# Optimization experiments

Measured on AMD Instinct MI355X. Metric: run time of the kernel, lower is better.

Reference implementation:

```python
import jax, jax.numpy as jnp
import numpy as np

B, S, H, E = 8, 2048, 1024, 8
CAP_FACTOR = 1.25  # deepspeed-style capacity factor for top-1 gating


def setup_inputs() -> dict:
    key = jax.random.key(0)
    ks = jax.random.split(key, 10)
    sc = 0.02
    return {
        "x": jax.random.normal(ks[0], (B, S, H), jnp.float32),
        "W_in": jax.random.normal(ks[1], (H, H), jnp.float32) * sc,
        "b_in": jnp.zeros((H,), jnp.float32),
        "W_gate": jax.random.normal(ks[2], (H, E), jnp.float32) * sc,
        "W1": jax.random.normal(ks[3], (E, H, H), jnp.float32) * sc,
        "b1": jnp.zeros((E, H), jnp.float32),
        "W2": jax.random.normal(ks[4], (E, H, H), jnp.float32) * sc,
        "b2": jnp.zeros((E, H), jnp.float32),
        "Wr1": jax.random.normal(ks[5], (H, H), jnp.float32) * sc,
        "br1": jnp.zeros((H,), jnp.float32),
        "Wr2": jax.random.normal(ks[6], (H, H), jnp.float32) * sc,
        "br2": jnp.zeros((H,), jnp.float32),
        "W_coef": jax.random.normal(ks[7], (H, 2), jnp.float32) * sc,
        "b_coef": jnp.zeros((2,), jnp.float32),
        "W_out": jax.random.normal(ks[8], (H, H), jnp.float32) * sc,
        "b_out": jnp.zeros((H,), jnp.float32),
    }


def _moe(x, W_gate, W1, b1, W2, b2, Wr1, br1, Wr2, br2, W_coef, b_coef):
    # x: [T, H] flattened tokens. Top-1 gating with capacity dropping + residual expert.
    T, Hd = x.shape
    nE = W_gate.shape[1]
    cap = int(np.ceil(CAP_FACTOR * T / nE))  # static under jit

    gates = jax.nn.softmax(x @ W_gate)                  # [T, E]
    eidx = jnp.argmax(gates, axis=-1)                    # [T]
    mask1 = jax.nn.one_hot(eidx, nE, dtype=x.dtype)      # [T, E]
    pos = jnp.cumsum(mask1, axis=0) - 1.0                # position within each expert
    pos_tok = jnp.take_along_axis(pos, eidx[:, None], 1)[:, 0].astype(jnp.int32)
    keep = (pos_tok < cap).astype(x.dtype)               # capacity drop mask
    gate_val = jnp.take_along_axis(gates, eidx[:, None], 1)[:, 0] * keep  # [T]
    slot = jnp.minimum(pos_tok, cap - 1)                 # safe slot index

    # scatter tokens into [E, cap, H] buffers (dropped tokens contribute zeros)
    disp = jnp.zeros((nE, cap, Hd), x.dtype).at[eidx, slot].add(x * keep[:, None])
    h = jax.nn.relu(jnp.einsum('ech,ehf->ecf', disp, W1) + b1[:, None, :])
    eo = jnp.einsum('ecf,efg->ecg', h, W2) + b2[:, None, :]
    moe_out = eo[eidx, slot] * gate_val[:, None]         # gather back; dropped -> 0

    # residual expert on all tokens, mixed with learned 2-way softmax coefficient
    res = jax.nn.relu(x @ Wr1 + br1) @ Wr2 + br2
    coef = jax.nn.softmax(x @ W_coef + b_coef)           # [T, 2]
    return moe_out * coef[:, :1] + res * coef[:, 1:]


def reference(x, W_in, b_in, W_gate, W1, b1, W2, b2, Wr1, br1, Wr2, br2,
              W_coef, b_coef, W_out, b_out):
    Bb, Ss, Hd = x.shape
    t = x.reshape(-1, Hd) @ W_in + b_in
    t = _moe(t, W_gate, W1, b1, W2, b2, Wr1, br1, Wr2, br2, W_coef, b_coef)
    t = t @ W_out + b_out
    return t.reshape(Bb, Ss, Hd)
```

## Files before the change

kernel.cpp:

```cpp
#include <hip/hip_runtime.h>
#include <cstdint>

#define T_TOK 16384
#define HD    1024
#define NE    8
#define CAP   2560
#define NCHUNK (T_TOK / 64)

typedef __attribute__((ext_vector_type(4))) float f32x4;
typedef __attribute__((ext_vector_type(8))) short bf16x8;

__device__ __forceinline__ unsigned short f2bf(float f) {
    union { float f; unsigned u; } x{f};
    unsigned r = x.u + 0x7FFF + ((x.u >> 16) & 1);
    return (unsigned short)(r >> 16);
}

__device__ __forceinline__ void gload_lds16(const unsigned short* g, unsigned short* l) {
    __builtin_amdgcn_global_load_lds(
        (const __attribute__((address_space(1))) void*)g,
        (__attribute__((address_space(3))) void*)l, 16, 0, 0);
}

template<bool GATHER, bool RELU, bool ROWSCALE, bool SCATTER, bool OUTBF16>
__global__ __launch_bounds__(512)
void gemm_bf16_k(const unsigned short* __restrict__ A,
                 const unsigned short* __restrict__ Bt,
                 const float* __restrict__ bias,
                 void* __restrict__ Cv,
                 int M, int N, int K,
                 const int* __restrict__ idxTab,
                 const float* __restrict__ rs,
                 const float* __restrict__ post,
                 long aB, long bB, long biasB, long tabB, long cB)
{
    const int nx = gridDim.x, ny = gridDim.y;
    long nwg = (long)nx * ny * gridDim.z;
    long flat = blockIdx.x + (long)nx * (blockIdx.y + (long)ny * blockIdx.z);
    long cpx = nwg >> 3;
    long swz = (flat & 7) * cpx + (flat >> 3);
    const int bx = (int)(swz % nx);
    const int by = (int)((swz / nx) % ny);
    const int bz = (int)(swz / ((long)nx * ny));

    A  += (long)bz * aB;
    Bt += (long)bz * bB;
    const float* bptr = bias ? bias + (long)bz * biasB : nullptr;
    const int* tab = idxTab ? idxTab + (long)bz * tabB : nullptr;
    float*          Cf = (float*)Cv + (long)bz * cB;
    unsigned short* Cb = (unsigned short*)Cv + (long)bz * cB;

    const int m0 = by * 256, n0 = bx * 128;

    if ((GATHER || SCATTER) && tab[m0] < 0) return;

    __shared__ unsigned short As[256][64];
    __shared__ unsigned short Bs[128][64];

    const int tid  = threadIdx.x;
    const int wv   = tid >> 6;
    const int lane = tid & 63;

    const int srow = lane >> 3;
    const int schk = lane & 7;

    const unsigned short* aSrc[4];
    const unsigned short* bSrc[2];
    #pragma unroll
    for (int i = 0; i < 4; ++i) {
        int lrow = wv * 32 + i * 8 + srow;
        int scol = ((schk ^ (lrow & 7)) * 8);
        long sr;
        if (GATHER) { int tr = tab[m0 + lrow]; sr = tr < 0 ? 0 : tr; }
        else        sr = m0 + lrow;
        aSrc[i] = A + sr * (long)K + scol;
    }
    #pragma unroll
    for (int i = 0; i < 2; ++i) {
        int lrow = wv * 16 + i * 8 + srow;
        int scol = ((schk ^ (lrow & 7)) * 8);
        bSrc[i] = Bt + (long)(n0 + lrow) * K + scol;
    }

    f32x4 acc[4][4] = {};
    const int wm = wv >> 1, wn = wv & 1;
    const int fr = lane & 15, kg = lane >> 4;

    for (int k0 = 0; k0 < K; k0 += 64) {
        __syncthreads();
        #pragma unroll
        for (int i = 0; i < 4; ++i)
            gload_lds16(aSrc[i] + k0, &As[wv * 32 + i * 8][0]);
        #pragma unroll
        for (int i = 0; i < 2; ++i)
            gload_lds16(bSrc[i] + k0, &Bs[wv * 16 + i * 8][0]);
        __syncthreads();

        #pragma unroll
        for (int kk = 0; kk < 2; ++kk) {
            bf16x8 af[4], bfr[4];
            #pragma unroll
            for (int i2 = 0; i2 < 4; ++i2) {
                int R = wm * 64 + i2 * 16 + fr;
                af[i2] = *(const bf16x8*)&As[R][((kk * 4 + kg) ^ (R & 7)) * 8];
            }
            #pragma unroll
            for (int j2 = 0; j2 < 4; ++j2) {
                int R = wn * 64 + j2 * 16 + fr;
                bfr[j2] = *(const bf16x8*)&Bs[R][((kk * 4 + kg) ^ (R & 7)) * 8];
            }
            #pragma unroll
            for (int i2 = 0; i2 < 4; ++i2)
                #pragma unroll
                for (int j2 = 0; j2 < 4; ++j2)
                    acc[i2][j2] = __builtin_amdgcn_mfma_f32_16x16x32_bf16(
                        af[i2], bfr[j2], acc[i2][j2], 0, 0, 0);
        }
    }

    const int colL = lane & 15, rgrp = (lane >> 4) * 4;
    #pragma unroll
    for (int i2 = 0; i2 < 4; ++i2) {
        #pragma unroll
        for (int r = 0; r < 4; ++r) {
            int gm = m0 + wm * 64 + i2 * 16 + rgrp + r;
            int token = gm; float sc = 1.0f;
            if (SCATTER) {
                token = tab[gm];
                if (token < 0) continue;
                sc = rs[token];
            } else if (ROWSCALE) {
                sc = rs[gm];
            }
            #pragma unroll
            for (int j2 = 0; j2 < 4; ++j2) {
                int gn = n0 + wn * 64 + j2 * 16 + colL;
                float v = acc[i2][j2][r] + (bptr ? bptr[gn] : 0.0f);
                if (RELU) v = fmaxf(v, 0.0f);
                if (SCATTER) {
                    Cf[(long)token * N + gn] += v * sc;
                } else {
                    if (ROWSCALE) {
                        v = v * sc + (post ? post[gn] : 0.0f);
                    }
                    if (OUTBF16) Cb[(long)gm * N + gn] = f2bf(v);
                    else         Cf[(long)gm * N + gn] = v;
                }
            }
        }
    }
}

__global__ __launch_bounds__(256)
void cast_bf16_k(const float* __restrict__ in, unsigned short* __restrict__ out,
                 long n4)
{
    long i = (long)blockIdx.x * 256 + threadIdx.x;
    long stride = (long)gridDim.x * 256;
    for (; i < n4; i += stride) {
        float4 v = ((const float4*)in)[i];
        ushort4 o;
        o.x = f2bf(v.x); o.y = f2bf(v.y); o.z = f2bf(v.z); o.w = f2bf(v.w);
        ((ushort4*)out)[i] = o;
    }
}

__global__ __launch_bounds__(256)
void transpose_cast_k(const float* __restrict__ W, unsigned short* __restrict__ Wt,
                      int K, int N, long wB, long wtB)
{
    const int z = blockIdx.z;
    W  += (long)z * wB;
    Wt += (long)z * wtB;
    __shared__ float tile[64][65];
    const int k0 = blockIdx.x * 64, n0 = blockIdx.y * 64;
    const int c = threadIdx.x & 63, r4 = threadIdx.x >> 6;
    #pragma unroll 4
    for (int it = 0; it < 16; ++it) {
        int row = it * 4 + r4;
        tile[row][c] = W[(long)(k0 + row) * N + n0 + c];
    }
    __syncthreads();
    #pragma unroll 4
    for (int it = 0; it < 16; ++it) {
        int nrow = it * 4 + r4;
        Wt[(long)(n0 + nrow) * K + k0 + c] = f2bf(tile[c][nrow]);
    }
}

__global__ void vecmat_init_k(const float* __restrict__ badd, long bB,
                              float* __restrict__ out, long oB)
{
    const int z = blockIdx.y;
    const int n = blockIdx.x * 256 + threadIdx.x;
    out[z * oB + n] = badd ? badd[z * bB + n] : 0.0f;
}

__global__ void vecmat_acc_k(const float* __restrict__ v, long vB,
                             const float* __restrict__ W, long wB,
                             float* __restrict__ out, long oB)
{
    const int z = blockIdx.z;
    const int n = blockIdx.x * 256 + threadIdx.x;
    const int kc = blockIdx.y;
    const float* vp = v + z * vB;
    const float* Wp = W + z * wB;
    float acc = 0.f;
    #pragma unroll 8
    for (int k = kc * 128; k < kc * 128 + 128; ++k)
        acc = fmaf(vp[k], Wp[(long)k * HD + n], acc);
    atomicAdd(out + z * oB + n, acc);
}

__global__ __launch_bounds__(256)
void wsmall_k(const float* __restrict__ W_in, const float* __restrict__ W_gate,
              const float* __restrict__ W_coef,
              float* __restrict__ wgp, float* __restrict__ wcp)
{
    const int r = blockIdx.x * 4 + (threadIdx.x >> 6);
    const int lane = threadIdx.x & 63;
    float s[10] = {};
    for (int k = lane; k < HD; k += 64) {
        float a = W_in[(long)r * HD + k];
        const float4* g = (const float4*)(W_gate + (long)k * 8);
        float4 g0 = g[0], g1 = g[1];
        s[0] += a * g0.x; s[1] += a * g0.y; s[2] += a * g0.z; s[3] += a * g0.w;
        s[4] += a * g1.x; s[5] += a * g1.y; s[6] += a * g1.z; s[7] += a * g1.w;
        float2 cv = *(const float2*)(W_coef + (long)k * 2);
        s[8] += a * cv.x; s[9] += a * cv.y;
    }
    #pragma unroll
    for (int off = 32; off > 0; off >>= 1)
        #pragma unroll
        for (int e = 0; e < 10; ++e) s[e] += __shfl_xor(s[e], off);
    if (lane == 0) {
        #pragma unroll
        for (int e = 0; e < 8; ++e) wgp[(long)r * 8 + e] = s[e];
        wcp[(long)r * 2 + 0] = s[8];
        wcp[(long)r * 2 + 1] = s[9];
    }
}

__global__ void gbias_k(const float* __restrict__ b_in, const float* __restrict__ W_gate,
                        const float* __restrict__ W_coef, const float* __restrict__ b_coef,
                        float* __restrict__ bg, float* __restrict__ bc)
{
    const int lane = threadIdx.x;
    float s[10] = {};
    for (int k = lane; k < HD; k += 64) {
        float a = b_in[k];
        const float4* g = (const float4*)(W_gate + (long)k * 8);
        float4 g0 = g[0], g1 = g[1];
        s[0] += a * g0.x; s[1] += a * g0.y; s[2] += a * g0.z; s[3] += a * g0.w;
        s[4] += a * g1.x; s[5] += a * g1.y; s[6] += a * g1.z; s[7] += a * g1.w;
        float2 cv = *(const float2*)(W_coef + (long)k * 2);
        s[8] += a * cv.x; s[9] += a * cv.y;
    }
    #pragma unroll
    for (int off = 32; off > 0; off >>= 1)
        #pragma unroll
        for (int e = 0; e < 10; ++e) s[e] += __shfl_xor(s[e], off);
    if (lane == 0) {
        #pragma unroll
        for (int e = 0; e < 8; ++e) bg[e] = s[e];
        bc[0] = s[8] + b_coef[0];
        bc[1] = s[9] + b_coef[1];
    }
}

__global__ __launch_bounds__(256)
void gating_k(const float* __restrict__ x,
              const float* __restrict__ Wg,
              const float* __restrict__ Wc,
              const float* __restrict__ bg,
              const float* __restrict__ bc,
              unsigned short* __restrict__ xb,
              int* __restrict__ eidx,
              float* __restrict__ gval,
              float* __restrict__ coef0,
              float* __restrict__ coef1)
{
    const int tok = (blockIdx.x * 256 + threadIdx.x) >> 6;
    const int lane = threadIdx.x & 63;
    const float* row = x + (long)tok * HD;
    unsigned short* orow = xb + (long)tok * HD;

    float acc[8] = {};
    float c0 = 0.f, c1 = 0.f;
    for (int i = 0; i < HD / 64; ++i) {
        int k = i * 64 + lane;
        float tv = row[k];
        orow[k] = f2bf(tv);
        const float4* wg = (const float4*)(Wg + (long)k * 8);
        float4 w0 = wg[0], w1 = wg[1];
        acc[0] = fmaf(tv, w0.x, acc[0]); acc[1] = fmaf(tv, w0.y, acc[1]);
        acc[2] = fmaf(tv, w0.z, acc[2]); acc[3] = fmaf(tv, w0.w, acc[3]);
        acc[4] = fmaf(tv, w1.x, acc[4]); acc[5] = fmaf(tv, w1.y, acc[5]);
        acc[6] = fmaf(tv, w1.z, acc[6]); acc[7] = fmaf(tv, w1.w, acc[7]);
        float2 wcv = *(const float2*)(Wc + (long)k * 2);
        c0 = fmaf(tv, wcv.x, c0);
        c1 = fmaf(tv, wcv.y, c1);
    }
    #pragma unroll
    for (int off = 32; off > 0; off >>= 1) {
        #pragma unroll
        for (int e = 0; e < 8; ++e) acc[e] += __shfl_xor(acc[e], off);
        c0 += __shfl_xor(c0, off);
        c1 += __shfl_xor(c1, off);
    }
    if (lane == 0) {
        #pragma unroll
        for (int e = 0; e < 8; ++e) acc[e] += bg[e];
        float m = acc[0]; int best = 0;
        #pragma unroll
        for (int e = 1; e < 8; ++e) if (acc[e] > m) { m = acc[e]; best = e; }
        float s = 0.f;
        #pragma unroll
        for (int e = 0; e < 8; ++e) s += expf(acc[e] - m);
        eidx[tok] = best;
        gval[tok] = 1.0f / s;
        float l0 = c0 + bc[0], l1 = c1 + bc[1];
        float mm = fmaxf(l0, l1);
        float e0 = expf(l0 - mm), e1 = expf(l1 - mm);
        float inv = 1.0f / (e0 + e1);
        coef0[tok] = e0 * inv;
        coef1[tok] = e1 * inv;
    }
}

__global__ void scan_hist_k(const int* __restrict__ eidx,
                            int* __restrict__ counts,
                            int* __restrict__ idxTab)
{
    const int b = blockIdx.x;
    const int lane = threadIdx.x;
    for (int j = b * 64 + lane; j < NE * CAP; j += NCHUNK * 64)
        idxTab[j] = -1;
    int e = eidx[b * 64 + lane];
    #pragma unroll
    for (int ex = 0; ex < NE; ++ex) {
        unsigned long long msk = __ballot(e == ex);
        if (lane == ex) counts[b * NE + ex] = (int)__popcll(msk);
    }
}

__global__ void scan_offsets_k(const int* __restrict__ counts,
                               int* __restrict__ offsets)
{
    const int e = threadIdx.x;
    if (e < NE) {
        int run = 0;
        for (int b = 0; b < NCHUNK; ++b) {
            offsets[b * NE + e] = run;
            run += counts[b * NE + e];
        }
    }
}

__global__ void scan_fill_k(const int* __restrict__ eidx,
                            const float* __restrict__ gval,
                            const float* __restrict__ coef0,
                            const int* __restrict__ offsets,
                            int* __restrict__ idxTab,
                            float* __restrict__ smoe)
{
    const int b = blockIdx.x;
    const int lane = threadIdx.x;
    const int tok = b * 64 + lane;
    int e = eidx[tok];
    unsigned long long below = (lane == 0) ? 0ull : ((~0ull) >> (64 - lane));
    int myrank = 0;
    #pragma unroll
    for (int ex = 0; ex < NE; ++ex) {
        unsigned long long msk = __ballot(e == ex);
        if (e == ex) myrank = (int)__popcll(msk & below) + offsets[b * NE + ex];
    }
    if (myrank < CAP) {
        idxTab[e * CAP + myrank] = tok;
        smoe[tok] = gval[tok] * coef0[tok];
    } else {
        smoe[tok] = 0.0f;
    }
}

extern "C" void kernel_launch(void* const* d_in, const int* in_sizes, int n_in,
                              void* d_out, int out_size, void* d_ws, size_t ws_size,
                              hipStream_t stream)
{
    const float* x      = (const float*)d_in[0];
    const float* W_in   = (const float*)d_in[1];
    const float* b_in   = (const float*)d_in[2];
    const float* W_gate = (const float*)d_in[3];
    const float* W1     = (const float*)d_in[4];
    const float* b1     = (const float*)d_in[5];
    const float* W2     = (const float*)d_in[6];
    const float* b2     = (const float*)d_in[7];
    const float* Wr1    = (const float*)d_in[8];
    const float* br1    = (const float*)d_in[9];
    const float* Wr2    = (const float*)d_in[10];
    const float* br2    = (const float*)d_in[11];
    const float* W_coef = (const float*)d_in[12];
    const float* b_coef = (const float*)d_in[13];
    const float* W_out  = (const float*)d_in[14];
    const float* b_out  = (const float*)d_in[15];
    float* out = (float*)d_out;

    const size_t MiB = 1024 * 1024;
    char* ws = (char*)d_ws;
    unsigned short* W1T   = (unsigned short*)(ws + 0);
    unsigned short* Wr1T  = (unsigned short*)(ws + 16 * MiB);
    unsigned short* Winp  = (unsigned short*)(ws + 18 * MiB);
    unsigned short* Wr2p  = (unsigned short*)(ws + 20 * MiB);
    unsigned short* W2p   = (unsigned short*)(ws + 22 * MiB);
    unsigned short* WoutT = (unsigned short*)(ws + 38 * MiB);
    unsigned short* h     = (unsigned short*)(ws + 0);
    unsigned short* WF1T  = (unsigned short*)(ws + 40 * MiB);
    unsigned short* WFr1T = (unsigned short*)(ws + 56 * MiB);
    unsigned short* WFr2T = (unsigned short*)(ws + 58 * MiB);
    unsigned short* WF2T  = (unsigned short*)(ws + 60 * MiB);
    unsigned short* res1  = (unsigned short*)(ws + 76 * MiB);
    char* sm = ws + 108 * MiB;
    float* wgp  = (float*)(sm);            sm += HD * 8 * 4;
    float* wcp  = (float*)(sm);            sm += HD * 2 * 4;
    float* bg   = (float*)(sm);            sm += 64;
    float* bc   = (float*)(sm);            sm += 64;
    float* bf1  = (float*)(sm);            sm += NE * HD * 4;
    float* bfr1 = (float*)(sm);            sm += HD * 4;
    float* c2   = (float*)(sm);            sm += HD * 4;
    float* c3   = (float*)(sm);            sm += NE * HD * 4;
    int*   eidx = (int*)(sm);              sm += T_TOK * 4;
    float* gval = (float*)(sm);            sm += T_TOK * 4;
    float* cf0  = (float*)(sm);            sm += T_TOK * 4;
    float* cf1  = (float*)(sm);            sm += T_TOK * 4;
    float* smoe = (float*)(sm);            sm += T_TOK * 4;
    int* idxTab = (int*)(sm);              sm += NE * CAP * 4;
    int* counts = (int*)(sm);              sm += NCHUNK * NE * 4;
    int* offs   = (int*)(sm);              sm += NCHUNK * NE * 4;
    unsigned short* xb = (unsigned short*)d_out;
    (void)ws_size; (void)in_sizes; (void)n_in; (void)out_size;

    const long HD2 = (long)HD * HD;
    dim3 blk(256);
    dim3 blkG(512);
    dim3 gT(16, 16, 1);
    dim3 gT8(16, 16, 8);
    dim3 gBig(HD / 128, T_TOK / 256, 1);
    dim3 gExp(HD / 128, CAP / 256, NE);
    dim3 gFuse(HD / 128, HD / 256, 9);

    transpose_cast_k<<<gT8, blk, 0, stream>>>(W1, W1T, HD, HD, HD2, HD2);
    transpose_cast_k<<<gT,  blk, 0, stream>>>(Wr1,   Wr1T,  HD, HD, 0, 0);
    transpose_cast_k<<<gT,  blk, 0, stream>>>(W_out, WoutT, HD, HD, 0, 0);
    cast_bf16_k<<<512,  blk, 0, stream>>>(W_in, Winp, HD2 / 4);
    cast_bf16_k<<<512,  blk, 0, stream>>>(Wr2,  Wr2p, HD2 / 4);
    cast_bf16_k<<<2048, blk, 0, stream>>>(W2,   W2p,  (long)NE * HD2 / 4);
    wsmall_k<<<HD / 4, blk, 0, stream>>>(W_in, W_gate, W_coef, wgp, wcp);
    gbias_k<<<1, 64, 0, stream>>>(b_in, W_gate, W_coef, b_coef, bg, bc);
    { dim3 gi(HD / 256, NE), ga(HD / 256, NE, NE);
      vecmat_init_k<<<dim3(HD/256, NE), blk, 0, stream>>>(b1, HD, bf1, HD);
      vecmat_acc_k <<<dim3(HD/256, 8, NE), blk, 0, stream>>>(b_in, 0, W1, HD2, bf1, HD);
      vecmat_init_k<<<dim3(HD/256, 1), blk, 0, stream>>>(br1, 0, bfr1, 0);
      vecmat_acc_k <<<dim3(HD/256, 8, 1), blk, 0, stream>>>(b_in, 0, Wr1, 0, bfr1, 0);
      vecmat_init_k<<<dim3(HD/256, 1), blk, 0, stream>>>(nullptr, 0, c2, 0);
      vecmat_acc_k <<<dim3(HD/256, 8, 1), blk, 0, stream>>>(br2, 0, W_out, 0, c2, 0);
      vecmat_init_k<<<dim3(HD/256, NE), blk, 0, stream>>>(nullptr, 0, c3, HD);
      vecmat_acc_k <<<dim3(HD/256, 8, NE), blk, 0, stream>>>(b2, HD, W_out, 0, c3, HD);
    }
    gating_k<<<T_TOK / 4, blk, 0, stream>>>(x, wgp, wcp, bg, bc, xb,
                                            eidx, gval, cf0, cf1);
    scan_hist_k<<<NCHUNK, 64, 0, stream>>>(eidx, counts, idxTab);
    scan_offsets_k<<<1, 64, 0, stream>>>(counts, offs);
    scan_fill_k<<<NCHUNK, 64, 0, stream>>>(eidx, gval, cf0, offs, idxTab, smoe);
    gemm_bf16_k<false, false, false, false, true><<<gFuse, blkG, 0, stream>>>(
        W1T, Winp, nullptr, WF1T, HD, HD, HD, nullptr, nullptr, nullptr,
        HD2, 0, 0, 0, HD2);
    gemm_bf16_k<false, false, false, false, true><<<gFuse, blkG, 0, stream>>>(
        WoutT, Wr2p, nullptr, WFr2T, HD, HD, HD, nullptr, nullptr, nullptr,
        0, HD2, 0, 0, HD2);
    gemm_bf16_k<true, true, false, false, true><<<gExp, blkG, 0, stream>>>(
        xb, WF1T, bf1, h, CAP, HD, HD, idxTab, nullptr, nullptr,
        0, HD2, HD, CAP, (long)CAP * HD);
    gemm_bf16_k<false, true, false, false, true><<<gBig, blkG, 0, stream>>>(
        xb, WFr1T, bfr1, res1, T_TOK, HD, HD, nullptr, nullptr, nullptr,
        0, 0, 0, 0, 0);
    gemm_bf16_k<false, false, true, false, false><<<gBig, blkG, 0, stream>>>(
        res1, WFr2T, c2, out, T_TOK, HD, HD, nullptr, cf1, b_out,
        0, 0, 0, 0, 0);
    gemm_bf16_k<false, false, false, true, false><<<gExp, blkG, 0, stream>>>(
        h, WF2T, c3, out, CAP, HD, HD, idxTab, smoe, nullptr,
        (long)CAP * HD, HD2, HD, CAP, 0);
}
```

Measured before the change: 459.9 us.

## Unfold W_out from expert and residual weights; apply a separate output GEMM

Stops pre-multiplying W2 and Wr2 by W_out, which removes the 9-batch weight-fusion GEMM and the bias-folding vecmat kernels. The residual GEMM now writes a coefficient-scaled fp32 mix into the output buffer. The expert scatter GEMM adds its result to that mix and writes a bf16 copy, and a small kernel casts capacity-dropped tokens, collected through an atomic drop list. A final token-by-H GEMM with W_out then produces the output. This has more FLOPs than the folded weights and adds an extra pass over activations, in exchange for fewer preprocessing kernels and keeping W_out unfused, which may also improve numerical accuracy.

```diff
diff --git a/kernel.cpp b/kernel.cpp
--- a/kernel.cpp
+++ b/kernel.cpp
@@ -31,7 +31,7 @@
                  int M, int N, int K,
                  const int* __restrict__ idxTab,
                  const float* __restrict__ rs,
-                 const float* __restrict__ post,
+                 const float* __restrict__ addsrc,
                  long aB, long bB, long biasB, long tabB, long cB)
 {
     const int nx = gridDim.x, ny = gridDim.y;
@@ -138,16 +138,33 @@
                 float v = acc[i2][j2][r] + (bptr ? bptr[gn] : 0.0f);
                 if (RELU) v = fmaxf(v, 0.0f);
                 if (SCATTER) {
-                    Cf[(long)token * N + gn] += v * sc;
+                    long idx = (long)token * N + gn;
+                    if (OUTBF16) Cb[idx] = f2bf(addsrc[idx] + v * sc);
+                    else         Cf[idx] += v * sc;
                 } else {
-                    if (ROWSCALE) {
-                        v = v * sc + (post ? post[gn] : 0.0f);
-                    }
+                    if (ROWSCALE) v *= sc;
                     if (OUTBF16) Cb[(long)gm * N + gn] = f2bf(v);
                     else         Cf[(long)gm * N + gn] = v;
                 }
             }
         }
+    }
+}
+
+__global__ __launch_bounds__(256)
+void drop_cast_k(const float* __restrict__ mix, unsigned short* __restrict__ mixb,
+                 const int* __restrict__ droplist, const int* __restrict__ dropcnt)
+{
+    const int cnt = *dropcnt;
+    for (int i = blockIdx.x; i < cnt; i += gridDim.x) {
+        const int tok = droplist[i];
+        const float4* src = (const float4*)(mix + (long)tok * HD);
+        ushort4* dst = (ushort4*)(mixb + (long)tok * HD);
+        const int j = threadIdx.x;
+        float4 v = src[j];
+        ushort4 o;
+        o.x = f2bf(v.x); o.y = f2bf(v.y); o.z = f2bf(v.z); o.w = f2bf(v.w);
+        dst[j] = o;
     }
 }
 
@@ -345,9 +362,11 @@
 }
 
 __global__ void scan_offsets_k(const int* __restrict__ counts,
-                               int* __restrict__ offsets)
+                               int* __restrict__ offsets,
+                               int* __restrict__ dropcnt)
 {
     const int e = threadIdx.x;
+    if (e == 63) *dropcnt = 0;
     if (e < NE) {
         int run = 0;
         for (int b = 0; b < NCHUNK; ++b) {
@@ -362,7 +381,9 @@
                             const float* __restrict__ coef0,
                             const int* __restrict__ offsets,
                             int* __restrict__ idxTab,
-                            float* __restrict__ smoe)
+                            float* __restrict__ smoe,
+                            int* __restrict__ droplist,
+                            int* __restrict__ dropcnt)
 {
     const int b = blockIdx.x;
     const int lane = threadIdx.x;
@@ -380,6 +401,8 @@
         smoe[tok] = gval[tok] * coef0[tok];
     } else {
         smoe[tok] = 0.0f;
+        int di = atomicAdd(dropcnt, 1);
+        droplist[di] = tok;
     }
 }
 
@@ -410,24 +433,21 @@
     unsigned short* W1T   = (unsigned short*)(ws + 0);
     unsigned short* Wr1T  = (unsigned short*)(ws + 16 * MiB);
     unsigned short* Winp  = (unsigned short*)(ws + 18 * MiB);
-    unsigned short* Wr2p  = (unsigned short*)(ws + 20 * MiB);
-    unsigned short* W2p   = (unsigned short*)(ws + 22 * MiB);
-    unsigned short* WoutT = (unsigned short*)(ws + 38 * MiB);
     unsigned short* h     = (unsigned short*)(ws + 0);
     unsigned short* WF1T  = (unsigned short*)(ws + 40 * MiB);
     unsigned short* WFr1T = (unsigned short*)(ws + 56 * MiB);
-    unsigned short* WFr2T = (unsigned short*)(ws + 58 * MiB);
-    unsigned short* WF2T  = (unsigned short*)(ws + 60 * MiB);
-    unsigned short* res1  = (unsigned short*)(ws + 76 * MiB);
-    char* sm = ws + 108 * MiB;
+    unsigned short* W2T   = (unsigned short*)(ws + 58 * MiB);
+    unsigned short* Wr2T  = (unsigned short*)(ws + 74 * MiB);
+    unsigned short* WoutT = (unsigned short*)(ws + 76 * MiB);
+    unsigned short* res1  = (unsigned short*)(ws + 78 * MiB);
+    unsigned short* mixb  = (unsigned short*)(ws + 78 * MiB);
+    char* sm = ws + 110 * MiB;
     float* wgp  = (float*)(sm);            sm += HD * 8 * 4;
     float* wcp  = (float*)(sm);            sm += HD * 2 * 4;
     float* bg   = (float*)(sm);            sm += 64;
     float* bc   = (float*)(sm);            sm += 64;
     float* bf1  = (float*)(sm);            sm += NE * HD * 4;
     float* bfr1 = (float*)(sm);            sm += HD * 4;
-    float* c2   = (float*)(sm);            sm += HD * 4;
-    float* c3   = (float*)(sm);            sm += NE * HD * 4;
     int*   eidx = (int*)(sm);              sm += T_TOK * 4;
     float* gval = (float*)(sm);            sm += T_TOK * 4;
     float* cf0  = (float*)(sm);            sm += T_TOK * 4;
@@ -436,7 +456,10 @@
     int* idxTab = (int*)(sm);              sm += NE * CAP * 4;
     int* counts = (int*)(sm);              sm += NCHUNK * NE * 4;
     int* offs   = (int*)(sm);              sm += NCHUNK * NE * 4;
+    int* droplist = (int*)(sm);            sm += T_TOK * 4;
+    int* dropcnt  = (int*)(sm);            sm += 64;
     unsigned short* xb = (unsigned short*)d_out;
+    float* mix = out;
     (void)ws_size; (void)in_sizes; (void)n_in; (void)out_size;
 
     const long HD2 = (long)HD * HD;
@@ -450,33 +473,25 @@
 
     transpose_cast_k<<<gT8, blk, 0, stream>>>(W1, W1T, HD, HD, HD2, HD2);
     transpose_cast_k<<<gT,  blk, 0, stream>>>(Wr1,   Wr1T,  HD, HD, 0, 0);
+    transpose_cast_k<<<gT8, blk, 0, stream>>>(W2, W2T, HD, HD, HD2, HD2);
+    transpose_cast_k<<<gT,  blk, 0, stream>>>(Wr2,   Wr2T,  HD, HD, 0, 0);
     transpose_cast_k<<<gT,  blk, 0, stream>>>(W_out, WoutT, HD, HD, 0, 0);
-    cast_bf16_k<<<512,  blk, 0, stream>>>(W_in, Winp, HD2 / 4);
-    cast_bf16_k<<<512,  blk, 0, stream>>>(Wr2,  Wr2p, HD2 / 4);
-    cast_bf16_k<<<2048, blk, 0, stream>>>(W2,   W2p,  (long)NE * HD2 / 4);
+    cast_bf16_k<<<512, blk, 0, stream>>>(W_in, Winp, HD2 / 4);
     wsmall_k<<<HD / 4, blk, 0, stream>>>(W_in, W_gate, W_coef, wgp, wcp);
     gbias_k<<<1, 64, 0, stream>>>(b_in, W_gate, W_coef, b_coef, bg, bc);
-    { dim3 gi(HD / 256, NE), ga(HD / 256, NE, NE);
-      vecmat_init_k<<<dim3(HD/256, NE), blk, 0, stream>>>(b1, HD, bf1, HD);
-      vecmat_acc_k <<<dim3(HD/256, 8, NE), blk, 0, stream>>>(b_in, 0, W1, HD2, bf1, HD);
-      vecmat_init_k<<<dim3(HD/256, 1), blk, 0, stream>>>(br1, 0, bfr1, 0);
-      vecmat_acc_k <<<dim3(HD/256, 8, 1), blk, 0, stream>>>(b_in, 0, Wr1, 0, bfr1, 0);
-      vecmat_init_k<<<dim3(HD/256, 1), blk, 0, stream>>>(nullptr, 0, c2, 0);
-      vecmat_acc_k <<<dim3(HD/256, 8, 1), blk, 0, stream>>>(br2, 0, W_out, 0, c2, 0);
-      vecmat_init_k<<<dim3(HD/256, NE), blk, 0, stream>>>(nullptr, 0, c3, HD);
-      vecmat_acc_k <<<dim3(HD/256, 8, NE), blk, 0, stream>>>(b2, HD, W_out, 0, c3, HD);
-    }
+    vecmat_init_k<<<dim3(HD/256, NE), blk, 0, stream>>>(b1, HD, bf1, HD);
+    vecmat_acc_k <<<dim3(HD/256, 8, NE), blk, 0, stream>>>(b_in, 0, W1, HD2, bf1, HD);
+    vecmat_init_k<<<dim3(HD/256, 1), blk, 0, stream>>>(br1, 0, bfr1, 0);
+    vecmat_acc_k <<<dim3(HD/256, 8, 1), blk, 0, stream>>>(b_in, 0, Wr1, 0, bfr1, 0);
     gating_k<<<T_TOK / 4, blk, 0, stream>>>(x, wgp, wcp, bg, bc, xb,
                                             eidx, gval, cf0, cf1);
     scan_hist_k<<<NCHUNK, 64, 0, stream>>>(eidx, counts, idxTab);
-    scan_offsets_k<<<1, 64, 0, stream>>>(counts, offs);
-    scan_fill_k<<<NCHUNK, 64, 0, stream>>>(eidx, gval, cf0, offs, idxTab, smoe);
+    scan_offsets_k<<<1, 64, 0, stream>>>(counts, offs, dropcnt);
+    scan_fill_k<<<NCHUNK, 64, 0, stream>>>(eidx, gval, cf0, offs, idxTab, smoe,
+                                           droplist, dropcnt);
     gemm_bf16_k<false, false, false, false, true><<<gFuse, blkG, 0, stream>>>(
         W1T, Winp, nullptr, WF1T, HD, HD, HD, nullptr, nullptr, nullptr,
         HD2, 0, 0, 0, HD2);
-    gemm_bf16_k<false, false, false, false, true><<<gFuse, blkG, 0, stream>>>(
-        WoutT, Wr2p, nullptr, WFr2T, HD, HD, HD, nullptr, nullptr, nullptr,
-        0, HD2, 0, 0, HD2);
     gemm_bf16_k<true, true, false, false, true><<<gExp, blkG, 0, stream>>>(
         xb, WF1T, bf1, h, CAP, HD, HD, idxTab, nullptr, nullptr,
         0, HD2, HD, CAP, (long)CAP * HD);
@@ -484,9 +499,13 @@
         xb, WFr1T, bfr1, res1, T_TOK, HD, HD, nullptr, nullptr, nullptr,
         0, 0, 0, 0, 0);
     gemm_bf16_k<false, false, true, false, false><<<gBig, blkG, 0, stream>>>(
-        res1, WFr2T, c2, out, T_TOK, HD, HD, nullptr, cf1, b_out,
+        res1, Wr2T, br2, mix, T_TOK, HD, HD, nullptr, cf1, nullptr,
         0, 0, 0, 0, 0);
-    gemm_bf16_k<false, false, false, true, false><<<gExp, blkG, 0, stream>>>(
-        h, WF2T, c3, out, CAP, HD, HD, idxTab, smoe, nullptr,
+    gemm_bf16_k<false, false, false, true, true><<<gExp, blkG, 0, stream>>>(
+        h, W2T, b2, mixb, CAP, HD, HD, idxTab, smoe, mix,
         (long)CAP * HD, HD2, HD, CAP, 0);
-}
+    drop_cast_k<<<256, blk, 0, stream>>>(mix, mixb, droplist, dropcnt);
+    gemm_bf16_k<false, false, false, false, false><<<gBig, blkG, 0, stream>>>(
+        mixb, WoutT, b_out, out, T_TOK, HD, HD, nullptr, nullptr, nullptr,
+        0, 0, 0, 0, 0);
+}
```

Result: no change. 459.5 us (-0.1%).

## Unfold W_out from expert and residual weights; add final output GEMM over bf16 mix

Applied to the files above, without the earlier changes.

Stops precomposing W_out into W2 and Wr2 via fused weight GEMMs and bias vecmats. The residual and expert down-projections now write a bf16 mixed buffer (expert scatter does a bf16 read-modify-write), and a separate token-wide GEMM applies W_out and b_out. This removes the per-call weight-fusion GEMMs and bias precompute but adds a full T×H×H GEMM and rounds the intermediate to bf16.

```diff
diff --git a/kernel.cpp b/kernel.cpp
--- a/kernel.cpp
+++ b/kernel.cpp
@@ -14,6 +14,12 @@
     union { float f; unsigned u; } x{f};
     unsigned r = x.u + 0x7FFF + ((x.u >> 16) & 1);
     return (unsigned short)(r >> 16);
+}
+
+__device__ __forceinline__ float bf2f(unsigned short b) {
+    union { unsigned u; float f; } x;
+    x.u = ((unsigned)b) << 16;
+    return x.f;
 }
 
 __device__ __forceinline__ void gload_lds16(const unsigned short* g, unsigned short* l) {
@@ -31,7 +37,6 @@
                  int M, int N, int K,
                  const int* __restrict__ idxTab,
                  const float* __restrict__ rs,
-                 const float* __restrict__ post,
                  long aB, long bB, long biasB, long tabB, long cB)
 {
     const int nx = gridDim.x, ny = gridDim.y;
@@ -138,11 +143,14 @@
                 float v = acc[i2][j2][r] + (bptr ? bptr[gn] : 0.0f);
                 if (RELU) v = fmaxf(v, 0.0f);
                 if (SCATTER) {
-                    Cf[(long)token * N + gn] += v * sc;
+                    long idx = (long)token * N + gn;
+                    if (OUTBF16) {
+                        Cb[idx] = f2bf(bf2f(Cb[idx]) + v * sc);
+                    } else {
+                        Cf[idx] += v * sc;
+                    }
                 } else {
-                    if (ROWSCALE) {
-                        v = v * sc + (post ? post[gn] : 0.0f);
-                    }
+                    if (ROWSCALE) v *= sc;
                     if (OUTBF16) Cb[(long)gm * N + gn] = f2bf(v);
                     else         Cf[(long)gm * N + gn] = v;
                 }
@@ -410,24 +418,21 @@
     unsigned short* W1T   = (unsigned short*)(ws + 0);
     unsigned short* Wr1T  = (unsigned short*)(ws + 16 * MiB);
     unsigned short* Winp  = (unsigned short*)(ws + 18 * MiB);
-    unsigned short* Wr2p  = (unsigned short*)(ws + 20 * MiB);
-    unsigned short* W2p   = (unsigned short*)(ws + 22 * MiB);
-    unsigned short* WoutT = (unsigned short*)(ws + 38 * MiB);
     unsigned short* h     = (unsigned short*)(ws + 0);
     unsigned short* WF1T  = (unsigned short*)(ws + 40 * MiB);
     unsigned short* WFr1T = (unsigned short*)(ws + 56 * MiB);
-    unsigned short* WFr2T = (unsigned short*)(ws + 58 * MiB);
-    unsigned short* WF2T  = (unsigned short*)(ws + 60 * MiB);
-    unsigned short* res1  = (unsigned short*)(ws + 76 * MiB);
-    char* sm = ws + 108 * MiB;
+    unsigned short* W2T   = (unsigned short*)(ws + 58 * MiB);
+    unsigned short* Wr2T  = (unsigned short*)(ws + 74 * MiB);
+    unsigned short* WoutT = (unsigned short*)(ws + 76 * MiB);
+    unsigned short* res1  = (unsigned short*)(ws + 78 * MiB);
+    unsigned short* mixb  = (unsigned short*)(ws + 110 * MiB);
+    char* sm = ws + 142 * MiB;
     float* wgp  = (float*)(sm);            sm += HD * 8 * 4;
     float* wcp  = (float*)(sm);            sm += HD * 2 * 4;
     float* bg   = (float*)(sm);            sm += 64;
     float* bc   = (float*)(sm);            sm += 64;
     float* bf1  = (float*)(sm);            sm += NE * HD * 4;
     float* bfr1 = (float*)(sm);            sm += HD * 4;
-    float* c2   = (float*)(sm);            sm += HD * 4;
-    float* c3   = (float*)(sm);            sm += NE * HD * 4;
     int*   eidx = (int*)(sm);              sm += T_TOK * 4;
     float* gval = (float*)(sm);            sm += T_TOK * 4;
     float* cf0  = (float*)(sm);            sm += T_TOK * 4;
@@ -450,43 +455,37 @@
 
     transpose_cast_k<<<gT8, blk, 0, stream>>>(W1, W1T, HD, HD, HD2, HD2);
     transpose_cast_k<<<gT,  blk, 0, stream>>>(Wr1,   Wr1T,  HD, HD, 0, 0);
+    transpose_cast_k<<<gT8, blk, 0, stream>>>(W2, W2T, HD, HD, HD2, HD2);
+    transpose_cast_k<<<gT,  blk, 0, stream>>>(Wr2,   Wr2T,  HD, HD, 0, 0);
     transpose_cast_k<<<gT,  blk, 0, stream>>>(W_out, WoutT, HD, HD, 0, 0);
-    cast_bf16_k<<<512,  blk, 0, stream>>>(W_in, Winp, HD2 / 4);
-    cast_bf16_k<<<512,  blk, 0, stream>>>(Wr2,  Wr2p, HD2 / 4);
-    cast_bf16_k<<<2048, blk, 0, stream>>>(W2,   W2p,  (long)NE * HD2 / 4);
+    cast_bf16_k<<<512, blk, 0, stream>>>(W_in, Winp, HD2 / 4);
     wsmall_k<<<HD / 4, blk, 0, stream>>>(W_in, W_gate, W_coef, wgp, wcp);
     gbias_k<<<1, 64, 0, stream>>>(b_in, W_gate, W_coef, b_coef, bg, bc);
-    { dim3 gi(HD / 256, NE), ga(HD / 256, NE, NE);
-      vecmat_init_k<<<dim3(HD/256, NE), blk, 0, stream>>>(b1, HD, bf1, HD);
-      vecmat_acc_k <<<dim3(HD/256, 8, NE), blk, 0, stream>>>(b_in, 0, W1, HD2, bf1, HD);
-      vecmat_init_k<<<dim3(HD/256, 1), blk, 0, stream>>>(br1, 0, bfr1, 0);
-      vecmat_acc_k <<<dim3(HD/256, 8, 1), blk, 0, stream>>>(b_in, 0, Wr1, 0, bfr1, 0);
-      vecmat_init_k<<<dim3(HD/256, 1), blk, 0, stream>>>(nullptr, 0, c2, 0);
-      vecmat_acc_k <<<dim3(HD/256, 8, 1), blk, 0, stream>>>(br2, 0, W_out, 0, c2, 0);
-      vecmat_init_k<<<dim3(HD/256, NE), blk, 0, stream>>>(nullptr, 0, c3, HD);
-      vecmat_acc_k <<<dim3(HD/256, 8, NE), blk, 0, stream>>>(b2, HD, W_out, 0, c3, HD);
-    }
+    vecmat_init_k<<<dim3(HD/256, NE), blk, 0, stream>>>(b1, HD, bf1, HD);
+    vecmat_acc_k <<<dim3(HD/256, 8, NE), blk, 0, stream>>>(b_in, 0, W1, HD2, bf1, HD);
+    vecmat_init_k<<<dim3(HD/256, 1), blk, 0, stream>>>(br1, 0, bfr1, 0);
+    vecmat_acc_k <<<dim3(HD/256, 8, 1), blk, 0, stream>>>(b_in, 0, Wr1, 0, bfr1, 0);
     gating_k<<<T_TOK / 4, blk, 0, stream>>>(x, wgp, wcp, bg, bc, xb,
                                             eidx, gval, cf0, cf1);
     scan_hist_k<<<NCHUNK, 64, 0, stream>>>(eidx, counts, idxTab);
     scan_offsets_k<<<1, 64, 0, stream>>>(counts, offs);
     scan_fill_k<<<NCHUNK, 64, 0, stream>>>(eidx, gval, cf0, offs, idxTab, smoe);
     gemm_bf16_k<false, false, false, false, true><<<gFuse, blkG, 0, stream>>>(
-        W1T, Winp, nullptr, WF1T, HD, HD, HD, nullptr, nullptr, nullptr,
+        W1T, Winp, nullptr, WF1T, HD, HD, HD, nullptr, nullptr,
         HD2, 0, 0, 0, HD2);
-    gemm_bf16_k<false, false, false, false, true><<<gFuse, blkG, 0, stream>>>(
-        WoutT, Wr2p, nullptr, WFr2T, HD, HD, HD, nullptr, nullptr, nullptr,
-        0, HD2, 0, 0, HD2);
     gemm_bf16_k<true, true, false, false, true><<<gExp, blkG, 0, stream>>>(
-        xb, WF1T, bf1, h, CAP, HD, HD, idxTab, nullptr, nullptr,
+        xb, WF1T, bf1, h, CAP, HD, HD, idxTab, nullptr,
         0, HD2, HD, CAP, (long)CAP * HD);
     gemm_bf16_k<false, true, false, false, true><<<gBig, blkG, 0, stream>>>(
-        xb, WFr1T, bfr1, res1, T_TOK, HD, HD, nullptr, nullptr, nullptr,
+        xb, WFr1T, bfr1, res1, T_TOK, HD, HD, nullptr, nullptr,
         0, 0, 0, 0, 0);
-    gemm_bf16_k<false, false, true, false, false><<<gBig, blkG, 0, stream>>>(
-        res1, WFr2T, c2, out, T_TOK, HD, HD, nullptr, cf1, b_out,
+    gemm_bf16_k<false, false, true, false, true><<<gBig, blkG, 0, stream>>>(
+        res1, Wr2T, br2, mixb, T_TOK, HD, HD, nullptr, cf1,
         0, 0, 0, 0, 0);
-    gemm_bf16_k<false, false, false, true, false><<<gExp, blkG, 0, stream>>>(
-        h, WF2T, c3, out, CAP, HD, HD, idxTab, smoe, nullptr,
+    gemm_bf16_k<false, false, false, true, true><<<gExp, blkG, 0, stream>>>(
+        h, W2T, b2, mixb, CAP, HD, HD, idxTab, smoe,
         (long)CAP * HD, HD2, HD, CAP, 0);
-}
+    gemm_bf16_k<false, false, false, false, false><<<gBig, blkG, 0, stream>>>(
+        mixb, WoutT, b_out, out, T_TOK, HD, HD, nullptr, nullptr,
+        0, 0, 0, 0, 0);
+}
```

Measured after the change: 450.3 us. 2.1% less time.
